# Optimization experiments

Hardware: AMD Instinct MI355X
Metric: run time of the kernel (lower is better)

## Reference

```python
import jax, jax.numpy as jnp
import numpy as np

B, T, C = 2, 4096, 768
H = 12
D = C // H  # head_dim = 64


def setup_inputs() -> dict:
    key = jax.random.key(0)
    k1, k2, k3 = jax.random.split(key, 3)
    x = jax.random.normal(k1, (B, T, C), dtype=jnp.float32)
    Wqkv = jax.random.normal(k2, (C, 3 * C), dtype=jnp.float32) * (C ** -0.5)
    Wproj = jax.random.normal(k3, (C, C), dtype=jnp.float32) * (C ** -0.5)
    bproj = jnp.zeros((C,), dtype=jnp.float32)
    return {"x": x, "Wqkv": Wqkv, "Wproj": Wproj, "bproj": bproj}


def reference(x, Wqkv, Wproj, bproj):
    b, t, c = x.shape
    # qkv projection (no bias), split into heads: [3, B, H, T, D]
    qkv = (x @ Wqkv).reshape(b, t, 3, H, D).transpose(2, 0, 3, 1, 4)
    q, k, v = qkv[0], qkv[1], qkv[2]
    scale = D ** -0.5
    # full causal score matrix [B, H, T, T] (faithful to naive impl)
    scores = jnp.einsum('bhqd,bhkd->bhqk', q, k) * scale
    causal = jnp.tril(jnp.ones((t, t), dtype=bool))
    scores = jnp.where(causal[None, None], scores, -jnp.inf)
    attn = jax.nn.softmax(scores, axis=-1)
    out = jnp.einsum('bhqk,bhkd->bhqd', attn, v)
    out = out.transpose(0, 2, 1, 3).reshape(b, t, c)
    return out @ Wproj + bproj
```

## Files before the change

### kernel.cpp

```cpp
#include <hip/hip_runtime.h>

#define B_ 2
#define T_ 4096
#define C_ 768
#define H_ 12
#define D_ 64
#define NTASK 768
#define QTASK 96

typedef __attribute__((ext_vector_type(8))) short bf16x8;
typedef __attribute__((ext_vector_type(4))) float f32x4;
typedef __attribute__((ext_vector_type(16))) float f32x16;

__device__ __forceinline__ unsigned short f2bf(float f) {
  union { float f; unsigned u; } v; v.f = f;
  unsigned r = v.u + 0x7fffu + ((v.u >> 16) & 1u);
  return (unsigned short)(r >> 16);
}

__device__ __forceinline__ float exp2_hw(float x) {
  float r;
  asm("v_exp_f32 %0, %1" : "=v"(r) : "v"(x));
  return r;
}

__device__ __forceinline__ void gll16(const void* g, void* l) {
  __builtin_amdgcn_global_load_lds((const __attribute__((address_space(1))) void*)g,
                                   (__attribute__((address_space(3))) void*)l, 16, 0, 0);
}


__global__ __launch_bounds__(256) void cast_bf16_k(const float* __restrict__ in,
                                                   unsigned short* __restrict__ out, int n4) {
  int i = blockIdx.x * 256 + threadIdx.x;
  if (i >= n4) return;
  float4 v = ((const float4*)in)[i];
  union { unsigned short s[4]; unsigned long long u; } o;
  o.s[0] = f2bf(v.x); o.s[1] = f2bf(v.y); o.s[2] = f2bf(v.z); o.s[3] = f2bf(v.w);
  ((unsigned long long*)out)[i] = o.u;
}

__global__ __launch_bounds__(256) void tcast_bf16_k(const float* __restrict__ in,
                                                    unsigned short* __restrict__ out,
                                                    int R, int C, unsigned* cnt) {
  int idx = blockIdx.x * 256 + threadIdx.x;
  if (cnt != nullptr && idx < 128) cnt[idx] = 0u;
  if (idx >= R * C) return;
  int r = idx / C, c = idx - r * C;
  out[(size_t)c * R + r] = f2bf(in[idx]);
}


#define QSCALE 0.1803368801111243f

template <int MODE>
__global__ __launch_bounds__(256) void gemm_k(const unsigned short* __restrict__ A,
                                              const unsigned short* __restrict__ Bt,
                                              int K,
                                              unsigned short* __restrict__ q_out,
                                              unsigned short* __restrict__ k_out,
                                              unsigned short* __restrict__ vt_out,
                                              float* __restrict__ f_out,
                                              const float* __restrict__ bias) {
  __shared__ short a_lds[128 * 32];
  __shared__ short b_lds[128 * 32];
  const int tid = threadIdx.x;
  const int wave = tid >> 6, lane = tid & 63;
  const int wm = wave >> 1, wn = wave & 1;
  const int lr = lane & 15, lc = lane >> 4;
  const int m0 = blockIdx.x * 128, n0 = blockIdx.y * 128;

  f32x4 acc[4][4];
  for (int mi = 0; mi < 4; ++mi)
    for (int ni = 0; ni < 4; ++ni) acc[mi][ni] = (f32x4){0.f, 0.f, 0.f, 0.f};

  for (int k0 = 0; k0 < K; k0 += 32) {
    __syncthreads();
    for (int p = 0; p < 2; ++p) {
      int chunk = p * 256 + wave * 64 + lane;
      int r = chunk >> 2, cc = chunk & 3;
      int c = cc ^ ((r >> 1) & 3);
      int base = (p * 256 + wave * 64) * 8;
      gll16(A + (size_t)(m0 + r) * K + k0 + c * 8, a_lds + base);
      gll16(Bt + (size_t)(n0 + r) * K + k0 + c * 8, b_lds + base);
    }
    __syncthreads();
    bf16x8 af[4], bfrag[4];
    for (int mi = 0; mi < 4; ++mi) {
      int r = wm * 64 + mi * 16 + lr;
      af[mi] = *(const bf16x8*)&a_lds[r * 32 + (lc ^ ((r >> 1) & 3)) * 8];
    }
    for (int ni = 0; ni < 4; ++ni) {
      int r = wn * 64 + ni * 16 + lr;
      bfrag[ni] = *(const bf16x8*)&b_lds[r * 32 + (lc ^ ((r >> 1) & 3)) * 8];
    }
    for (int mi = 0; mi < 4; ++mi)
      for (int ni = 0; ni < 4; ++ni)
        acc[mi][ni] = __builtin_amdgcn_mfma_f32_16x16x32_bf16(af[mi], bfrag[ni], acc[mi][ni], 0, 0, 0);
  }

  if (MODE == 0) {
    for (int mi = 0; mi < 4; ++mi)
      for (int ni = 0; ni < 4; ++ni) {
        int nn = n0 + wn * 64 + ni * 16 + lr;
        int which = nn / 768;
        int rem = nn - which * 768;
        int h = rem >> 6, d = rem & 63;
        for (int r = 0; r < 4; ++r) {
          int m = m0 + wm * 64 + mi * 16 + lc * 4 + r;
          int b = m >> 12, t = m & (T_ - 1);
          float av = acc[mi][ni][r];
          if (which == 0) av *= QSCALE;
          unsigned short val = f2bf(av);
          size_t bh = (size_t)(b * H_ + h);
          if (which == 0)      q_out[(bh * T_ + t) * D_ + d] = val;
          else if (which == 1) k_out[(bh * T_ + t) * D_ + d] = val;
          else                 vt_out[(bh * D_ + d) * T_ + t] = val;
        }
      }
  } else {
    for (int mi = 0; mi < 4; ++mi)
      for (int ni = 0; ni < 4; ++ni) {
        int nn = n0 + wn * 64 + ni * 16 + lr;
        float bv = bias[nn];
        for (int r = 0; r < 4; ++r) {
          int m = m0 + wm * 64 + mi * 16 + lc * 4 + r;
          f_out[(size_t)m * C_ + nn] = acc[mi][ni][r] + bv;
        }
      }
  }
}


#define PACK8(SV, O)                                                              \
  do {                                                                            \
    unsigned w0, w1, w2, w3, w4, w5, w6, w7;                                      \
    asm("v_cvt_pk_bf16_f32 %0, %1, %2" : "=v"(w0) : "v"(SV[0]), "v"(SV[1]));      \
    asm("v_cvt_pk_bf16_f32 %0, %1, %2" : "=v"(w1) : "v"(SV[2]), "v"(SV[3]));      \
    asm("v_cvt_pk_bf16_f32 %0, %1, %2" : "=v"(w2) : "v"(SV[4]), "v"(SV[5]));      \
    asm("v_cvt_pk_bf16_f32 %0, %1, %2" : "=v"(w3) : "v"(SV[6]), "v"(SV[7]));      \
    asm("v_cvt_pk_bf16_f32 %0, %1, %2" : "=v"(w4) : "v"(SV[8]), "v"(SV[9]));      \
    asm("v_cvt_pk_bf16_f32 %0, %1, %2" : "=v"(w5) : "v"(SV[10]), "v"(SV[11]));    \
    asm("v_cvt_pk_bf16_f32 %0, %1, %2" : "=v"(w6) : "v"(SV[12]), "v"(SV[13]));    \
    asm("v_cvt_pk_bf16_f32 %0, %1, %2" : "=v"(w7) : "v"(SV[14]), "v"(SV[15]));    \
    asm("v_permlane32_swap_b32 %0, %1" : "+v"(w0), "+v"(w2));                     \
    asm("v_permlane32_swap_b32 %0, %1" : "+v"(w1), "+v"(w3));                     \
    asm("v_permlane32_swap_b32 %0, %1" : "+v"(w4), "+v"(w6));                     \
    asm("v_permlane32_swap_b32 %0, %1" : "+v"(w5), "+v"(w7));                     \
    pw[(O) + 0] = w0; pw[(O) + 1] = w1; pw[(O) + 2] = w2; pw[(O) + 3] = w3;       \
    pw[(O) + 4] = w4; pw[(O) + 5] = w5; pw[(O) + 6] = w6; pw[(O) + 7] = w7;       \
  } while (0)

__global__ __launch_bounds__(256) void flash4_k(const unsigned short* __restrict__ Qg,
                                                const unsigned short* __restrict__ Kg,
                                                const unsigned short* __restrict__ Vtg,
                                                unsigned short* __restrict__ Og,
                                                unsigned* __restrict__ cnt) {
  __shared__ short k_lds[2][8 * 512];
  __shared__ short vt_lds[2][8 * 512];
  __shared__ int task_s;

  const int tid = threadIdx.x;
  const int wave = tid >> 6, lane = tid & 63;
  const int lq = lane & 31;
  const int xq = blockIdx.x & 7;
  unsigned* myq = cnt + xq * 16;

  for (;;) {
    if (tid == 0) task_s = (int)atomicAdd(myq, 1u);
    __syncthreads();
    const int task = task_s;
    if (task >= QTASK) return;

    const int qi = 31 - task / 3;
    const int bh = xq * 3 + (task - (task / 3) * 3);
    const int qw = qi * 128 + wave * 32;
    const int q_g = qw + lq;

    const size_t kbase = (size_t)bh * T_ * D_;
    const size_t vbase = (size_t)bh * D_ * T_;

    const unsigned short* qrow = Qg + kbase + (size_t)q_g * D_;
    bf16x8 qf[4];
#pragma unroll
    for (int t = 0; t < 4; ++t) qf[t] = *(const bf16x8*)(qrow + t * 16 + (lane >> 5) * 8);

    f32x16 accT0, accT1;
#pragma unroll
    for (int r = 0; r < 16; ++r) { accT0[r] = 0.f; accT1[r] = 0.f; }
    float m = -INFINITY, l = 0.f;

    const int nt = 2 * qi + 2;

    auto stage = [&](int it, int buf) {
      const int kv = it * 64;
#pragma unroll
      for (int p = 0; p < 2; ++p) {
        int f = p * 4 + wave;
        int th = f >> 1, hf = f & 1;
        gll16(Kg + kbase + (size_t)(kv + hf * 32 + lq) * D_ + th * 16 + (lane >> 5) * 8,
              &k_lds[buf][f * 512]);
        gll16(Vtg + vbase + (size_t)(hf * 32 + lq) * T_ + kv + th * 16 + (lane >> 5) * 8,
              &vt_lds[buf][f * 512]);
      }
    };

    stage(0, 0);

    for (int it = 0; it < nt; ++it) {
      const int kv = it * 64;
      const int buf = it & 1;

      __builtin_amdgcn_s_barrier();
      __builtin_amdgcn_sched_barrier(0);
      if (it + 1 < nt) {
        stage(it + 1, buf ^ 1);
        asm volatile("s_waitcnt vmcnt(4)" ::: "memory");
      } else {
        asm volatile("s_waitcnt vmcnt(0)" ::: "memory");
      }
      __builtin_amdgcn_sched_barrier(0);
      __builtin_amdgcn_s_barrier();
      __builtin_amdgcn_sched_barrier(0);

      if (kv <= qw + 31) {
        f32x16 s0, s1;
#pragma unroll
        for (int r = 0; r < 16; ++r) { s0[r] = 0.f; s1[r] = 0.f; }
        __builtin_amdgcn_s_setprio(1);
#pragma unroll
        for (int t = 0; t < 4; ++t) {
          bf16x8 kf0 = *(const bf16x8*)&k_lds[buf][(t * 2 + 0) * 512 + lane * 8];
          bf16x8 kf1 = *(const bf16x8*)&k_lds[buf][(t * 2 + 1) * 512 + lane * 8];
          s0 = __builtin_amdgcn_mfma_f32_32x32x16_bf16(kf0, qf[t], s0, 0, 0, 0);
          s1 = __builtin_amdgcn_mfma_f32_32x32x16_bf16(kf1, qf[t], s1, 0, 0, 0);
        }
        __builtin_amdgcn_s_setprio(0);

        const int hi = lane >> 5;
        if (kv + 63 > qw) {
#pragma unroll
          for (int r = 0; r < 16; ++r) {
            int key0 = kv + ((r & 3) + 8 * (r >> 2) + 4 * hi);
            if (key0 > q_g) s0[r] = -INFINITY;
            if (key0 + 32 > q_g) s1[r] = -INFINITY;
          }
        }

        float mx[16];
#pragma unroll
        for (int r = 0; r < 16; ++r) mx[r] = fmaxf(s0[r], s1[r]);
#pragma unroll
        for (int st = 8; st >= 1; st >>= 1)
#pragma unroll
          for (int r = 0; r < 8; ++r) {
            if (r < st) mx[r] = fmaxf(mx[r], mx[r + st]);
          }
        float rx = fmaxf(mx[0], __shfl_xor(mx[0], 32));
        if (!__all(rx <= m + 8.f)) {
          float mn = fmaxf(m, rx);
          float al = exp2_hw(m - mn);
          m = mn;
          l *= al;
#pragma unroll
          for (int r = 0; r < 16; ++r) { accT0[r] *= al; accT1[r] *= al; }
        }
#pragma unroll
        for (int r = 0; r < 16; ++r) s0[r] = exp2_hw(s0[r] - m);
#pragma unroll
        for (int r = 0; r < 16; ++r) s1[r] = exp2_hw(s1[r] - m);
        float sm[16];
#pragma unroll
        for (int r = 0; r < 16; ++r) sm[r] = s0[r] + s1[r];
#pragma unroll
        for (int st = 8; st >= 1; st >>= 1)
#pragma unroll
          for (int r = 0; r < 8; ++r) {
            if (r < st) sm[r] += sm[r + st];
          }
        l += sm[0] + __shfl_xor(sm[0], 32);

        unsigned pw[16];
        PACK8(s0, 0);
        PACK8(s1, 8);

        __builtin_amdgcn_s_setprio(1);
#pragma unroll
        for (int ks = 0; ks < 4; ++ks) {
          union { unsigned u[4]; bf16x8 v; } pb;
          pb.u[0] = pw[ks * 4 + 0]; pb.u[1] = pw[ks * 4 + 1];
          pb.u[2] = pw[ks * 4 + 2]; pb.u[3] = pw[ks * 4 + 3];
          bf16x8 vf0 = *(const bf16x8*)&vt_lds[buf][(ks * 2 + 0) * 512 + lane * 8];
          bf16x8 vf1 = *(const bf16x8*)&vt_lds[buf][(ks * 2 + 1) * 512 + lane * 8];
          accT0 = __builtin_amdgcn_mfma_f32_32x32x16_bf16(vf0, pb.v, accT0, 0, 0, 0);
          accT1 = __builtin_amdgcn_mfma_f32_32x32x16_bf16(vf1, pb.v, accT1, 0, 0, 0);
        }
        __builtin_amdgcn_s_setprio(0);
      }
    }

    const float inv = 1.0f / l;
    const int b = bh / H_, h = bh - b * H_;
    const int hi = lane >> 5;
    unsigned short* orow = Og + ((size_t)b * T_ + q_g) * C_ + h * D_;
#pragma unroll
    for (int g = 0; g < 4; ++g) {
      int d0 = 8 * g + 4 * hi;
      float a0 = accT0[4 * g + 0] * inv, a1 = accT0[4 * g + 1] * inv;
      float a2 = accT0[4 * g + 2] * inv, a3 = accT0[4 * g + 3] * inv;
      float b0 = accT1[4 * g + 0] * inv, b1 = accT1[4 * g + 1] * inv;
      float b2 = accT1[4 * g + 2] * inv, b3 = accT1[4 * g + 3] * inv;
      uint2 ua, ub;
      asm("v_cvt_pk_bf16_f32 %0, %1, %2" : "=v"(ua.x) : "v"(a0), "v"(a1));
      asm("v_cvt_pk_bf16_f32 %0, %1, %2" : "=v"(ua.y) : "v"(a2), "v"(a3));
      asm("v_cvt_pk_bf16_f32 %0, %1, %2" : "=v"(ub.x) : "v"(b0), "v"(b1));
      asm("v_cvt_pk_bf16_f32 %0, %1, %2" : "=v"(ub.y) : "v"(b2), "v"(b3));
      *(uint2*)(orow + d0) = ua;
      *(uint2*)(orow + 32 + d0) = ub;
    }
    __syncthreads();
  }
}


extern "C" void kernel_launch(void* const* d_in, const int* in_sizes, int n_in,
                              void* d_out, int out_size, void* d_ws, size_t ws_size,
                              hipStream_t stream) {
  const float* x     = (const float*)d_in[0];
  const float* Wqkv  = (const float*)d_in[1];
  const float* Wproj = (const float*)d_in[2];
  const float* bproj = (const float*)d_in[3];
  float* out = (float*)d_out;

  char* ws = (char*)d_ws;
  unsigned short* xbf   = (unsigned short*)(ws);
  unsigned short* wqkvt = (unsigned short*)(ws + 12582912);
  unsigned short* wprjt = (unsigned short*)(ws + 16121856);
  unsigned short* Qb    = (unsigned short*)(ws + 17301504);
  unsigned short* Kb    = (unsigned short*)(ws + 29884416);
  unsigned short* Vtb   = (unsigned short*)(ws + 42467328);
  unsigned*       cnt   = (unsigned*)(ws + 55050240);

  cast_bf16_k<<<6144, 256, 0, stream>>>(x, xbf, (B_ * T_ * C_) / 4);
  tcast_bf16_k<<<(C_ * 3 * C_) / 256, 256, 0, stream>>>(Wqkv, wqkvt, C_, 3 * C_, cnt);
  tcast_bf16_k<<<(C_ * C_) / 256, 256, 0, stream>>>(Wproj, wprjt, C_, C_, nullptr);

  gemm_k<0><<<dim3((B_ * T_) / 128, (3 * C_) / 128), 256, 0, stream>>>(
      xbf, wqkvt, C_, Qb, Kb, Vtb, nullptr, nullptr);

  flash4_k<<<768, 256, 0, stream>>>(Qb, Kb, Vtb, xbf, cnt);

  gemm_k<1><<<dim3((B_ * T_) / 128, C_ / 128), 256, 0, stream>>>(
      xbf, wprjt, C_, nullptr, nullptr, nullptr, out, bproj);
}
```

Before: 231.3 us.

## Double-buffer GEMM, tile weight transpose, defer softmax sums, remap blocks

Several independent changes land together. The GEMM gains double-buffered LDS with async prefetch, XCD-aware block remapping and vectorized V^T stores. The weight transpose/cast becomes an LDS-tiled, coalesced kernel, and the counter reset moves into the x cast kernel. The flash kernel folds -m into the score accumulator init, defers row-sum reduction to a per-lane vector summed at the end, simplifies max reduction, and launches more persistent blocks. These aim to cut GEMM load latency, uncoalesced transpose writes and softmax reduction ALU work, at the cost of more LDS and extra complexity.

```diff
diff --git a/kernel.cpp b/kernel.cpp
--- a/kernel.cpp
+++ b/kernel.cpp
@@ -5,7 +5,6 @@
 #define C_ 768
 #define H_ 12
 #define D_ 64
-#define NTASK 768
 #define QTASK 96
 
 typedef __attribute__((ext_vector_type(8))) short bf16x8;
@@ -31,8 +30,10 @@
 
 
 __global__ __launch_bounds__(256) void cast_bf16_k(const float* __restrict__ in,
-                                                   unsigned short* __restrict__ out, int n4) {
+                                                   unsigned short* __restrict__ out, int n4,
+                                                   unsigned* __restrict__ cnt) {
   int i = blockIdx.x * 256 + threadIdx.x;
+  if (i < 128) cnt[i] = 0u;
   if (i >= n4) return;
   float4 v = ((const float4*)in)[i];
   union { unsigned short s[4]; unsigned long long u; } o;
@@ -40,14 +41,23 @@
   ((unsigned long long*)out)[i] = o.u;
 }
 
-__global__ __launch_bounds__(256) void tcast_bf16_k(const float* __restrict__ in,
+__global__ __launch_bounds__(256) void tpose_cast_k(const float* __restrict__ in,
                                                     unsigned short* __restrict__ out,
-                                                    int R, int C, unsigned* cnt) {
-  int idx = blockIdx.x * 256 + threadIdx.x;
-  if (cnt != nullptr && idx < 128) cnt[idx] = 0u;
-  if (idx >= R * C) return;
-  int r = idx / C, c = idx - r * C;
-  out[(size_t)c * R + r] = f2bf(in[idx]);
+                                                    int R, int C) {
+  __shared__ unsigned short t[64][65];
+  const int c0 = blockIdx.x * 64, r0 = blockIdx.y * 64;
+  const int tr = threadIdx.x >> 6, tc = threadIdx.x & 63;
+#pragma unroll
+  for (int i = 0; i < 16; ++i) {
+    int r = i * 4 + tr;
+    t[r][tc] = f2bf(in[(size_t)(r0 + r) * C + c0 + tc]);
+  }
+  __syncthreads();
+#pragma unroll
+  for (int i = 0; i < 16; ++i) {
+    int c = i * 4 + tr;
+    out[(size_t)(c0 + c) * R + r0 + tc] = t[tc][c];
+  }
 }
 
 
@@ -62,67 +72,120 @@
                                               unsigned short* __restrict__ vt_out,
                                               float* __restrict__ f_out,
                                               const float* __restrict__ bias) {
-  __shared__ short a_lds[128 * 32];
-  __shared__ short b_lds[128 * 32];
+  __shared__ short a_lds[2][128 * 32];
+  __shared__ short b_lds[2][128 * 32];
   const int tid = threadIdx.x;
   const int wave = tid >> 6, lane = tid & 63;
   const int wm = wave >> 1, wn = wave & 1;
   const int lr = lane & 15, lc = lane >> 4;
-  const int m0 = blockIdx.x * 128, n0 = blockIdx.y * 128;
+
+  const int id = blockIdx.x;
+  const int xcd = id & 7, idc = id >> 3;
+  const int bx = xcd * 8 + (idc & 7);
+  const int by = idc >> 3;
+  const int m0 = bx * 128, n0 = by * 128;
 
   f32x4 acc[4][4];
   for (int mi = 0; mi < 4; ++mi)
     for (int ni = 0; ni < 4; ++ni) acc[mi][ni] = (f32x4){0.f, 0.f, 0.f, 0.f};
 
-  for (int k0 = 0; k0 < K; k0 += 32) {
-    __syncthreads();
-    for (int p = 0; p < 2; ++p) {
-      int chunk = p * 256 + wave * 64 + lane;
-      int r = chunk >> 2, cc = chunk & 3;
-      int c = cc ^ ((r >> 1) & 3);
-      int base = (p * 256 + wave * 64) * 8;
-      gll16(A + (size_t)(m0 + r) * K + k0 + c * 8, a_lds + base);
-      gll16(Bt + (size_t)(n0 + r) * K + k0 + c * 8, b_lds + base);
+  const unsigned short *ap[2], *bp[2];
+  int lb[2];
+#pragma unroll
+  for (int p = 0; p < 2; ++p) {
+    int chunk = p * 256 + wave * 64 + lane;
+    int r = chunk >> 2, cc = chunk & 3;
+    int c = cc ^ ((r >> 1) & 3);
+    ap[p] = A + (size_t)(m0 + r) * K + c * 8;
+    bp[p] = Bt + (size_t)(n0 + r) * K + c * 8;
+    lb[p] = (p * 256 + wave * 64) * 8;
+  }
+
+  const int nks = K >> 5;
+#pragma unroll
+  for (int p = 0; p < 2; ++p) {
+    gll16(ap[p], &a_lds[0][lb[p]]);
+    gll16(bp[p], &b_lds[0][lb[p]]);
+    ap[p] += 32; bp[p] += 32;
+  }
+
+  for (int ks = 0; ks < nks; ++ks) {
+    const int buf = ks & 1;
+    __builtin_amdgcn_s_barrier();
+    __builtin_amdgcn_sched_barrier(0);
+    if (ks + 1 < nks) {
+#pragma unroll
+      for (int p = 0; p < 2; ++p) {
+        gll16(ap[p], &a_lds[buf ^ 1][lb[p]]);
+        gll16(bp[p], &b_lds[buf ^ 1][lb[p]]);
+        ap[p] += 32; bp[p] += 32;
+      }
+      asm volatile("s_waitcnt vmcnt(4)" ::: "memory");
+    } else {
+      asm volatile("s_waitcnt vmcnt(0)" ::: "memory");
     }
-    __syncthreads();
+    __builtin_amdgcn_sched_barrier(0);
+    __builtin_amdgcn_s_barrier();
+    __builtin_amdgcn_sched_barrier(0);
+
     bf16x8 af[4], bfrag[4];
+#pragma unroll
     for (int mi = 0; mi < 4; ++mi) {
       int r = wm * 64 + mi * 16 + lr;
-      af[mi] = *(const bf16x8*)&a_lds[r * 32 + (lc ^ ((r >> 1) & 3)) * 8];
+      af[mi] = *(const bf16x8*)&a_lds[buf][r * 32 + (lc ^ ((r >> 1) & 3)) * 8];
     }
+#pragma unroll
     for (int ni = 0; ni < 4; ++ni) {
       int r = wn * 64 + ni * 16 + lr;
-      bfrag[ni] = *(const bf16x8*)&b_lds[r * 32 + (lc ^ ((r >> 1) & 3)) * 8];
+      bfrag[ni] = *(const bf16x8*)&b_lds[buf][r * 32 + (lc ^ ((r >> 1) & 3)) * 8];
     }
+    __builtin_amdgcn_s_setprio(1);
+#pragma unroll
     for (int mi = 0; mi < 4; ++mi)
+#pragma unroll
       for (int ni = 0; ni < 4; ++ni)
         acc[mi][ni] = __builtin_amdgcn_mfma_f32_16x16x32_bf16(af[mi], bfrag[ni], acc[mi][ni], 0, 0, 0);
+    __builtin_amdgcn_s_setprio(0);
   }
 
   if (MODE == 0) {
+    const int nn0 = n0 + wn * 64 + lr;
+    const int which = n0 / 768;
+#pragma unroll
     for (int mi = 0; mi < 4; ++mi)
+#pragma unroll
       for (int ni = 0; ni < 4; ++ni) {
-        int nn = n0 + wn * 64 + ni * 16 + lr;
-        int which = nn / 768;
+        int nn = nn0 + ni * 16;
         int rem = nn - which * 768;
         int h = rem >> 6, d = rem & 63;
-        for (int r = 0; r < 4; ++r) {
-          int m = m0 + wm * 64 + mi * 16 + lc * 4 + r;
-          int b = m >> 12, t = m & (T_ - 1);
-          float av = acc[mi][ni][r];
-          if (which == 0) av *= QSCALE;
-          unsigned short val = f2bf(av);
-          size_t bh = (size_t)(b * H_ + h);
-          if (which == 0)      q_out[(bh * T_ + t) * D_ + d] = val;
-          else if (which == 1) k_out[(bh * T_ + t) * D_ + d] = val;
-          else                 vt_out[(bh * D_ + d) * T_ + t] = val;
+        int t0v = m0 + wm * 64 + mi * 16 + lc * 4;
+        int b = t0v >> 12, t = t0v & (T_ - 1);
+        size_t bh = (size_t)(b * H_ + h);
+        if (which == 2) {
+          unsigned u0, u1;
+          asm("v_cvt_pk_bf16_f32 %0, %1, %2" : "=v"(u0) : "v"(acc[mi][ni][0]), "v"(acc[mi][ni][1]));
+          asm("v_cvt_pk_bf16_f32 %0, %1, %2" : "=v"(u1) : "v"(acc[mi][ni][2]), "v"(acc[mi][ni][3]));
+          uint2 u = {u0, u1};
+          *(uint2*)&vt_out[(bh * D_ + d) * T_ + t] = u;
+        } else {
+#pragma unroll
+          for (int r = 0; r < 4; ++r) {
+            float av = acc[mi][ni][r];
+            if (which == 0) av *= QSCALE;
+            unsigned short val = f2bf(av);
+            if (which == 0) q_out[(bh * T_ + t + r) * D_ + d] = val;
+            else            k_out[(bh * T_ + t + r) * D_ + d] = val;
+          }
         }
       }
   } else {
+#pragma unroll
     for (int mi = 0; mi < 4; ++mi)
+#pragma unroll
       for (int ni = 0; ni < 4; ++ni) {
         int nn = n0 + wn * 64 + ni * 16 + lr;
         float bv = bias[nn];
+#pragma unroll
         for (int r = 0; r < 4; ++r) {
           int m = m0 + wm * 64 + mi * 16 + lc * 4 + r;
           f_out[(size_t)m * C_ + nn] = acc[mi][ni][r] + bv;
@@ -151,7 +214,7 @@
     pw[(O) + 4] = w4; pw[(O) + 5] = w5; pw[(O) + 6] = w6; pw[(O) + 7] = w7;       \
   } while (0)
 
-__global__ __launch_bounds__(256) void flash4_k(const unsigned short* __restrict__ Qg,
+__global__ __launch_bounds__(256) void flash5_k(const unsigned short* __restrict__ Qg,
                                                 const unsigned short* __restrict__ Kg,
                                                 const unsigned short* __restrict__ Vtg,
                                                 unsigned short* __restrict__ Og,
@@ -162,7 +225,7 @@
 
   const int tid = threadIdx.x;
   const int wave = tid >> 6, lane = tid & 63;
-  const int lq = lane & 31;
+  const int lq = lane & 31, hi = lane >> 5;
   const int xq = blockIdx.x & 7;
   unsigned* myq = cnt + xq * 16;
 
@@ -183,29 +246,26 @@
     const unsigned short* qrow = Qg + kbase + (size_t)q_g * D_;
     bf16x8 qf[4];
 #pragma unroll
-    for (int t = 0; t < 4; ++t) qf[t] = *(const bf16x8*)(qrow + t * 16 + (lane >> 5) * 8);
+    for (int t = 0; t < 4; ++t) qf[t] = *(const bf16x8*)(qrow + t * 16 + hi * 8);
 
     f32x16 accT0, accT1;
 #pragma unroll
     for (int r = 0; r < 16; ++r) { accT0[r] = 0.f; accT1[r] = 0.f; }
-    float m = -INFINITY, l = 0.f;
+    float lvec[16];
+#pragma unroll
+    for (int r = 0; r < 16; ++r) lvec[r] = 0.f;
+    float m = 0.f;
 
     const int nt = 2 * qi + 2;
 
-    auto stage = [&](int it, int buf) {
-      const int kv = it * 64;
-#pragma unroll
-      for (int p = 0; p < 2; ++p) {
-        int f = p * 4 + wave;
-        int th = f >> 1, hf = f & 1;
-        gll16(Kg + kbase + (size_t)(kv + hf * 32 + lq) * D_ + th * 16 + (lane >> 5) * 8,
-              &k_lds[buf][f * 512]);
-        gll16(Vtg + vbase + (size_t)(hf * 32 + lq) * T_ + kv + th * 16 + (lane >> 5) * 8,
-              &vt_lds[buf][f * 512]);
-      }
-    };
-
-    stage(0, 0);
+    const unsigned short* kp = Kg + kbase + (size_t)((wave & 1) * 32 + lq) * D_ + (wave >> 1) * 16 + hi * 8;
+    const unsigned short* vp = Vtg + vbase + (size_t)((wave & 1) * 32 + lq) * T_ + (wave >> 1) * 16 + hi * 8;
+    const int lb0 = wave * 512, lb1 = (wave + 4) * 512;
+
+    gll16(kp, &k_lds[0][lb0]); gll16(kp + 32, &k_lds[0][lb1]);
+    gll16(vp, &vt_lds[0][lb0]); gll16(vp + 32, &vt_lds[0][lb1]);
+    const unsigned short* kpn = kp + 64 * D_;
+    const unsigned short* vpn = vp + 64;
 
     for (int it = 0; it < nt; ++it) {
       const int kv = it * 64;
@@ -214,7 +274,9 @@
       __builtin_amdgcn_s_barrier();
       __builtin_amdgcn_sched_barrier(0);
       if (it + 1 < nt) {
-        stage(it + 1, buf ^ 1);
+        gll16(kpn, &k_lds[buf ^ 1][lb0]); gll16(kpn + 32, &k_lds[buf ^ 1][lb1]);
+        gll16(vpn, &vt_lds[buf ^ 1][lb0]); gll16(vpn + 32, &vt_lds[buf ^ 1][lb1]);
+        kpn += 64 * D_; vpn += 64;
         asm volatile("s_waitcnt vmcnt(4)" ::: "memory");
       } else {
         asm volatile("s_waitcnt vmcnt(0)" ::: "memory");
@@ -224,9 +286,10 @@
       __builtin_amdgcn_sched_barrier(0);
 
       if (kv <= qw + 31) {
+        const float negm = -m;
         f32x16 s0, s1;
 #pragma unroll
-        for (int r = 0; r < 16; ++r) { s0[r] = 0.f; s1[r] = 0.f; }
+        for (int r = 0; r < 16; ++r) { s0[r] = negm; s1[r] = negm; }
         __builtin_amdgcn_s_setprio(1);
 #pragma unroll
         for (int t = 0; t < 4; ++t) {
@@ -237,7 +300,6 @@
         }
         __builtin_amdgcn_s_setprio(0);
 
-        const int hi = lane >> 5;
         if (kv + 63 > qw) {
 #pragma unroll
           for (int r = 0; r < 16; ++r) {
@@ -250,35 +312,29 @@
         float mx[16];
 #pragma unroll
         for (int r = 0; r < 16; ++r) mx[r] = fmaxf(s0[r], s1[r]);
-#pragma unroll
-        for (int st = 8; st >= 1; st >>= 1)
-#pragma unroll
-          for (int r = 0; r < 8; ++r) {
-            if (r < st) mx[r] = fmaxf(mx[r], mx[r + st]);
-          }
-        float rx = fmaxf(mx[0], __shfl_xor(mx[0], 32));
-        if (!__all(rx <= m + 8.f)) {
-          float mn = fmaxf(m, rx);
-          float al = exp2_hw(m - mn);
-          m = mn;
-          l *= al;
-#pragma unroll
-          for (int r = 0; r < 16; ++r) { accT0[r] *= al; accT1[r] *= al; }
-        }
-#pragma unroll
-        for (int r = 0; r < 16; ++r) s0[r] = exp2_hw(s0[r] - m);
-#pragma unroll
-        for (int r = 0; r < 16; ++r) s1[r] = exp2_hw(s1[r] - m);
-        float sm[16];
-#pragma unroll
-        for (int r = 0; r < 16; ++r) sm[r] = s0[r] + s1[r];
-#pragma unroll
-        for (int st = 8; st >= 1; st >>= 1)
-#pragma unroll
-          for (int r = 0; r < 8; ++r) {
-            if (r < st) sm[r] += sm[r + st];
-          }
-        l += sm[0] + __shfl_xor(sm[0], 32);
+        float a0 = fmaxf(fmaxf(mx[0], mx[1]), mx[2]);
+        float a1 = fmaxf(fmaxf(mx[3], mx[4]), mx[5]);
+        float a2 = fmaxf(fmaxf(mx[6], mx[7]), mx[8]);
+        float a3 = fmaxf(fmaxf(mx[9], mx[10]), mx[11]);
+        float a4 = fmaxf(fmaxf(mx[12], mx[13]), mx[14]);
+        float rx = fmaxf(fmaxf(fmaxf(a0, a1), fmaxf(a2, a3)), fmaxf(a4, mx[15]));
+        rx = fmaxf(rx, __shfl_xor(rx, 32));
+
+        if (!__all(rx <= 8.f)) {
+          float dlt = fmaxf(rx, 0.f);
+          float al = exp2_hw(-dlt);
+          m += dlt;
+#pragma unroll
+          for (int r = 0; r < 16; ++r) { accT0[r] *= al; accT1[r] *= al; lvec[r] *= al; }
+#pragma unroll
+          for (int r = 0; r < 16; ++r) { s0[r] -= dlt; s1[r] -= dlt; }
+        }
+#pragma unroll
+        for (int r = 0; r < 16; ++r) s0[r] = exp2_hw(s0[r]);
+#pragma unroll
+        for (int r = 0; r < 16; ++r) s1[r] = exp2_hw(s1[r]);
+#pragma unroll
+        for (int r = 0; r < 16; ++r) lvec[r] += s0[r] + s1[r];
 
         unsigned pw[16];
         PACK8(s0, 0);
@@ -299,22 +355,25 @@
       }
     }
 
+    float l = 0.f;
+#pragma unroll
+    for (int r = 0; r < 16; ++r) l += lvec[r];
+    l += __shfl_xor(l, 32);
     const float inv = 1.0f / l;
     const int b = bh / H_, h = bh - b * H_;
-    const int hi = lane >> 5;
     unsigned short* orow = Og + ((size_t)b * T_ + q_g) * C_ + h * D_;
 #pragma unroll
     for (int g = 0; g < 4; ++g) {
       int d0 = 8 * g + 4 * hi;
-      float a0 = accT0[4 * g + 0] * inv, a1 = accT0[4 * g + 1] * inv;
-      float a2 = accT0[4 * g + 2] * inv, a3 = accT0[4 * g + 3] * inv;
-      float b0 = accT1[4 * g + 0] * inv, b1 = accT1[4 * g + 1] * inv;
-      float b2 = accT1[4 * g + 2] * inv, b3 = accT1[4 * g + 3] * inv;
+      float e0 = accT0[4 * g + 0] * inv, e1 = accT0[4 * g + 1] * inv;
+      float e2 = accT0[4 * g + 2] * inv, e3 = accT0[4 * g + 3] * inv;
+      float f0 = accT1[4 * g + 0] * inv, f1 = accT1[4 * g + 1] * inv;
+      float f2 = accT1[4 * g + 2] * inv, f3 = accT1[4 * g + 3] * inv;
       uint2 ua, ub;
-      asm("v_cvt_pk_bf16_f32 %0, %1, %2" : "=v"(ua.x) : "v"(a0), "v"(a1));
-      asm("v_cvt_pk_bf16_f32 %0, %1, %2" : "=v"(ua.y) : "v"(a2), "v"(a3));
-      asm("v_cvt_pk_bf16_f32 %0, %1, %2" : "=v"(ub.x) : "v"(b0), "v"(b1));
-      asm("v_cvt_pk_bf16_f32 %0, %1, %2" : "=v"(ub.y) : "v"(b2), "v"(b3));
+      asm("v_cvt_pk_bf16_f32 %0, %1, %2" : "=v"(ua.x) : "v"(e0), "v"(e1));
+      asm("v_cvt_pk_bf16_f32 %0, %1, %2" : "=v"(ua.y) : "v"(e2), "v"(e3));
+      asm("v_cvt_pk_bf16_f32 %0, %1, %2" : "=v"(ub.x) : "v"(f0), "v"(f1));
+      asm("v_cvt_pk_bf16_f32 %0, %1, %2" : "=v"(ub.y) : "v"(f2), "v"(f3));
       *(uint2*)(orow + d0) = ua;
       *(uint2*)(orow + 32 + d0) = ub;
     }
@@ -341,15 +400,15 @@
   unsigned short* Vtb   = (unsigned short*)(ws + 42467328);
   unsigned*       cnt   = (unsigned*)(ws + 55050240);
 
-  cast_bf16_k<<<6144, 256, 0, stream>>>(x, xbf, (B_ * T_ * C_) / 4);
-  tcast_bf16_k<<<(C_ * 3 * C_) / 256, 256, 0, stream>>>(Wqkv, wqkvt, C_, 3 * C_, cnt);
-  tcast_bf16_k<<<(C_ * C_) / 256, 256, 0, stream>>>(Wproj, wprjt, C_, C_, nullptr);
-
-  gemm_k<0><<<dim3((B_ * T_) / 128, (3 * C_) / 128), 256, 0, stream>>>(
+  cast_bf16_k<<<6144, 256, 0, stream>>>(x, xbf, (B_ * T_ * C_) / 4, cnt);
+  tpose_cast_k<<<dim3((3 * C_) / 64, C_ / 64), 256, 0, stream>>>(Wqkv, wqkvt, C_, 3 * C_);
+  tpose_cast_k<<<dim3(C_ / 64, C_ / 64), 256, 0, stream>>>(Wproj, wprjt, C_, C_);
+
+  gemm_k<0><<<(B_ * T_ / 128) * (3 * C_ / 128), 256, 0, stream>>>(
       xbf, wqkvt, C_, Qb, Kb, Vtb, nullptr, nullptr);
 
-  flash4_k<<<768, 256, 0, stream>>>(Qb, Kb, Vtb, xbf, cnt);
-
-  gemm_k<1><<<dim3((B_ * T_) / 128, C_ / 128), 256, 0, stream>>>(
+  flash5_k<<<1024, 256, 0, stream>>>(Qb, Kb, Vtb, xbf, cnt);
+
+  gemm_k<1><<<(B_ * T_ / 128) * (C_ / 128), 256, 0, stream>>>(
       xbf, wprjt, C_, nullptr, nullptr, nullptr, out, bproj);
 }
```

After: 197.5 us. 14.6% less time.
